# Optimization experiments

Hardware: AMD Instinct MI355X
Metric: run time of the kernel (lower is better)

## Reference

```python
import jax, jax.numpy as jnp
import numpy as np
from jax.scipy.special import logsumexp

R, B, D, V, F = 64, 64, 256, 32000, 7
DFF = 4 * D
K_ACT, TOPK_N, TOP_M = 6, 4, 2
NEG = -1e30
C_TAU = 0.20333333  # mean of (1 - alpha) over taus alpha in {0.5, 0.9, 0.99}; zero prev state


def _hex_neighbors(side=8):
    offs = [(1, 0), (-1, 0), (0, 1), (0, -1), (1, -1), (-1, 1)]
    idx = [[((r + dr) % side) * side + (c + dc) % side for dr, dc in offs]
           for r in range(side) for c in range(side)]
    return jnp.array(idx, dtype=jnp.int32)


def setup_inputs() -> dict:
    key = jax.random.key(0)
    ks = jax.random.split(key, 12)
    def rn(k, shp, s):
        return jax.random.normal(k, shp, dtype=jnp.float32) * s
    return {
        "x_per_region": rn(ks[0], (R, B, D), 1.0),
        "targets": jax.random.randint(ks[1], (B,), 0, V),
        "neighbor_indices": _hex_neighbors(8),
        "W1": rn(ks[2], (R, D, DFF), D ** -0.5),
        "b1": jnp.zeros((R, DFF), jnp.float32),
        "W2": rn(ks[3], (R, DFF, D), DFF ** -0.5),
        "b2": jnp.zeros((R, D), jnp.float32),
        "w_gate": rn(ks[4], (D,), D ** -0.5),
        "Wr": rn(ks[5], (D, D), D ** -0.5),
        "Wm": rn(ks[6], (D, D), D ** -0.5),
        "bm": jnp.zeros((D,), jnp.float32),
        "Wg": rn(ks[7], (D, F), D ** -0.5),
        "Wf": rn(ks[8], (F, D, V), 0.02),
        "e_fac": rn(ks[9], (F, D), 1.0),
        "Wb": rn(ks[10], (D, D), D ** -0.5),
    }


def reference(x_per_region, targets, neighbor_indices, W1, b1, W2, b2, w_gate,
              Wr, Wm, bm, Wg, Wf, e_fac, Wb):
    inv_sqrt_d = D ** -0.5
    # per-region FF (grouped GEMM over R regions), exact GELU as torch nn.GELU
    hid = jax.nn.gelu(jnp.einsum('rbd,rdf->rbf', x_per_region, W1) + b1[:, None, :],
                      approximate=False)
    h = jnp.einsum('rbf,rfd->rbd', hid, W2) + b2[:, None, :]
    s = C_TAU * h                    # multi-tau state update (zero prev state, zero neighbor msg)
    H = h + s                        # [R,B,D]
    # region sparsity gate: k-WTA over regions per batch element, io regions forced on
    sc_g = jnp.einsum('rbd,d->br', H, w_gate)           # [B,R]
    kth = jax.lax.top_k(sc_g, K_ACT)[0][:, -1]
    mask = (sc_g >= kth[:, None]).at[:, 0].set(True).at[:, R - 1].set(True)
    Hs = H * mask.T[:, :, None]
    # sparse message passing: top-k gated attention over hex neighbor list
    Nb = Hs[neighbor_indices]                           # [R,6,B,D]
    sc = jnp.einsum('rbd,rkbd->rkb', Hs, Nb) * inv_sqrt_d
    kthn = -jnp.sort(-sc, axis=1)[:, TOPK_N - 1]        # [R,B]
    w = jax.nn.softmax(jnp.where(sc >= kthn[:, None, :], sc, NEG), axis=1)
    H2 = Hs + jnp.einsum('rkb,rkbd->rbd', w, Nb) @ Wr
    # motor readout + multi-facet softmax (mixture over top-m facets)
    motor = H2[R - 1] @ Wm + bm                         # [B,D]
    g = motor @ Wg                                      # [B,F]
    gk = jax.lax.top_k(g, TOP_M)[0][:, -1]
    log_pi = jax.nn.log_softmax(jnp.where(g >= gk[:, None], g, NEG), axis=-1)
    lp = jax.nn.log_softmax(jnp.einsum('bd,fdv->bfv', motor, Wf), axis=-1)
    logp = logsumexp(log_pi[:, :, None] + lp, axis=1)   # [B,V]
    loss = -jnp.mean(jnp.take_along_axis(logp, targets[:, None], axis=1))
    # surprise-gated facet emitter + broadcast routing (next-step buffer, detached)
    S = jax.lax.stop_gradient(loss)
    boost = 1.0 + 2.0 * (S > 0.7).astype(H2.dtype)
    gb = jnp.einsum('rbd,df->rbf', H2, Wg)
    gbk = -jnp.sort(-gb, axis=-1)[..., TOP_M - 1]
    pi = jax.nn.softmax(jnp.where(gb >= gbk[..., None], gb, NEG), axis=-1)
    Bc = H2 * jnp.einsum('rbf,fd->rbd', pi, e_fac) * boost
    NbB = Bc[neighbor_indices]                          # [R,6,B,D]
    sc2 = jnp.einsum('rbd,rkbd->rkb', H2, NbB) * inv_sqrt_d
    kth2 = -jnp.sort(-sc2, axis=1)[:, TOPK_N - 1]
    w2 = jax.nn.softmax(jnp.where(sc2 >= kth2[:, None, :], sc2, NEG), axis=1)
    msg_next = jax.lax.stop_gradient(jnp.einsum('rkb,rkbd->rbd', w2, NbB) @ Wb)
    return logp, loss, msg_next
```

## Files before the change

kernel.cpp:

```cpp
#include <hip/hip_runtime.h>

#define RR 64
#define BB 64
#define DD 256
#define DFF_ 1024
#define VV 32000
#define FF 7

#define TIE_BAND(a, b) (2e-6 * (1.0 + 0.5 * (fabs(a) + fabs(b))))
#define BR_CLAMP 0.30f
#define TOT_CLAMP 0.19f

__device__ __forceinline__ float clampf(float x, float c) {
  return fminf(fmaxf(x, -c), c);
}


__global__ void t_hid(const float* __restrict__ x, const float* __restrict__ W1,
                      const float* __restrict__ b1, double* __restrict__ hid) {
  int fc = blockIdx.x, r = blockIdx.y;
  int t = threadIdx.x;
  int fg = t & 15, bg = t >> 4;
  __shared__ float xs[64][65];
  __shared__ float w1t[64][64];
  double acc[4][4];
#pragma unroll
  for (int i = 0; i < 4; ++i)
#pragma unroll
    for (int j = 0; j < 4; ++j) acc[i][j] = 0.0;
  const float* xr = x + (size_t)r * BB * DD;
  const float* w1r = W1 + (size_t)r * DD * DFF_;
  for (int dt = 0; dt < 4; ++dt) {
    for (int i = t; i < 4096; i += 256) {
      int d = i & 63, b = i >> 6;
      xs[d][b] = xr[b * DD + dt * 64 + d];
    }
    for (int i = t; i < 4096; i += 256) {
      int dd = i >> 6, ff = i & 63;
      w1t[dd][ff] = w1r[(size_t)(dt * 64 + dd) * DFF_ + fc * 64 + ff];
    }
    __syncthreads();
    for (int d = 0; d < 64; ++d) {
      double bv[4], wv[4];
#pragma unroll
      for (int i = 0; i < 4; ++i) bv[i] = (double)xs[d][bg * 4 + i];
#pragma unroll
      for (int j = 0; j < 4; ++j) wv[j] = (double)w1t[d][fg * 4 + j];
#pragma unroll
      for (int i = 0; i < 4; ++i)
#pragma unroll
        for (int j = 0; j < 4; ++j) acc[i][j] += bv[i] * wv[j];
    }
    __syncthreads();
  }
#pragma unroll
  for (int i = 0; i < 4; ++i) {
    int b = bg * 4 + i;
#pragma unroll
    for (int j = 0; j < 4; ++j) {
      int f = fc * 64 + fg * 4 + j;
      double v = acc[i][j] + (double)b1[r * DFF_ + f];
      hid[((size_t)(r * BB + b)) * DFF_ + f] =
          0.5 * v * (1.0 + erf(v * 0.70710678118654752440));
    }
  }
}

__global__ void t_H(const double* __restrict__ hid, const float* __restrict__ W2,
                    const float* __restrict__ b2, double* __restrict__ H) {
  int dc = blockIdx.x, bc = blockIdx.y, r = blockIdx.z;
  int t = threadIdx.x;
  int dg = t & 15, bg = t >> 4;
  __shared__ double ht[64][33];
  __shared__ float wt[64][32];
  double acc[2][2];
#pragma unroll
  for (int i = 0; i < 2; ++i)
#pragma unroll
    for (int j = 0; j < 2; ++j) acc[i][j] = 0.0;
  const double* hr = hid + (size_t)r * BB * DFF_;
  const float* w2r = W2 + (size_t)r * DFF_ * DD;
  for (int ft = 0; ft < 16; ++ft) {
    for (int i = t; i < 2048; i += 256) {
      int f = i & 63, b = i >> 6;
      ht[f][b] = hr[(size_t)(bc * 32 + b) * DFF_ + ft * 64 + f];
    }
    for (int i = t; i < 2048; i += 256) {
      int f = i >> 5, d = i & 31;
      wt[f][d] = w2r[(size_t)(ft * 64 + f) * DD + dc * 32 + d];
    }
    __syncthreads();
    for (int f = 0; f < 64; ++f) {
      double hb[2], wv[2];
#pragma unroll
      for (int i = 0; i < 2; ++i) hb[i] = ht[f][bg * 2 + i];
#pragma unroll
      for (int j = 0; j < 2; ++j) wv[j] = (double)wt[f][dg * 2 + j];
#pragma unroll
      for (int i = 0; i < 2; ++i)
#pragma unroll
        for (int j = 0; j < 2; ++j) acc[i][j] += hb[i] * wv[j];
    }
    __syncthreads();
  }
#pragma unroll
  for (int i = 0; i < 2; ++i) {
    int b = bc * 32 + bg * 2 + i;
#pragma unroll
    for (int j = 0; j < 2; ++j) {
      int d = dc * 32 + dg * 2 + j;
      double h = acc[i][j] + (double)b2[r * DD + d];
      H[((size_t)(r * BB + b)) * DD + d] = h + 0.20333333 * h;
    }
  }
}


__global__ void n_scg(const double* __restrict__ H, const float* __restrict__ wg,
                      double* __restrict__ scg) {
  __shared__ double hbuf[4][256];
  __shared__ float wgs[256];
  int t = threadIdx.x;
  int wv = t >> 6, lane = t & 63;
  int idx = blockIdx.x * 4 + wv;
  int r = idx >> 6, b = idx & 63;
  const double* hp = H + (size_t)idx * DD;
  wgs[t] = wg[t];
#pragma unroll
  for (int j = 0; j < 4; ++j) hbuf[wv][lane + j * 64] = hp[lane + j * 64];
  __syncthreads();
  if (lane == 0) {
    double a = 0.0;
    for (int d = 0; d < DD; ++d) a += hbuf[wv][d] * (double)wgs[d];
    scg[b * RR + r] = a;
  }
}

__global__ void n_mask_dual(const double* __restrict__ scg, float* __restrict__ maskH,
                            float* __restrict__ maskA, int* __restrict__ flagM) {
  int b = threadIdx.x;
  double v[64], w[64];
  for (int r = 0; r < RR; ++r) { v[r] = scg[b * RR + r]; w[r] = v[r]; }
  double k6 = 0.0, k7 = 0.0;
  int i6 = -1, i7 = -1;
  for (int it = 0; it < 7; ++it) {
    int mi = 0;
    for (int r = 1; r < RR; ++r) if (w[r] > w[mi]) mi = r;
    if (it == 5) { k6 = w[mi]; i6 = mi; }
    if (it == 6) { k7 = w[mi]; i7 = mi; }
    w[mi] = -INFINITY;
  }
  double gap = k6 - k7;
  int tie = (gap > 0.0 && gap < TIE_BAND(k6, k7)) ? 1 : 0;
  for (int r = 0; r < RR; ++r) {
    float mh = (v[r] >= k6 || r == 0 || r == RR - 1) ? 1.f : 0.f;
    maskH[b * RR + r] = mh;
    maskA[b * RR + r] = tie ? ((v[r] >= k7 || r == 0 || r == RR - 1) ? 1.f : 0.f) : mh;
    flagM[r * BB + b] = 0;
  }
  if (tie) {
    flagM[i6 * BB + b] = 1;
    flagM[i7 * BB + b] = 1;
  }
}

__global__ void n_hs(const double* __restrict__ H, const float* __restrict__ mask,
                     double* __restrict__ Hs) {
  int idx = blockIdx.x * 256 + threadIdx.x;
  int r = idx >> 14;
  int b = (idx >> 8) & 63;
  Hs[idx] = H[idx] * (double)mask[b * RR + r];
}

__global__ void n_hs_g(const double* __restrict__ H, const float* __restrict__ maskA,
                       const int* __restrict__ gate, double* __restrict__ HsM) {
  int rb = blockIdx.x;
  if (!gate[rb]) return;
  int t = threadIdx.x;
  size_t i = (size_t)rb * DD + t;
  int r = rb >> 6, b = rb & 63;
  HsM[i] = H[i] * (double)maskA[b * RR + r];
}

__global__ void n_w6x(const double* __restrict__ self, const double* __restrict__ nb,
                      const int* __restrict__ nidx, double* __restrict__ wout,
                      double* __restrict__ walt, int* __restrict__ flag) {
  __shared__ double sbuf[256];
  __shared__ double qbuf[6][256];
  int idx = blockIdx.x;
  int r = idx >> 6, b = idx & 63;
  int lane = threadIdx.x;
  const double* sp = self + (size_t)idx * DD;
#pragma unroll
  for (int j = 0; j < 4; ++j) sbuf[lane + j * 64] = sp[lane + j * 64];
  for (int k = 0; k < 6; ++k) {
    int nr = nidx[r * 6 + k];
    const double* qp = nb + ((size_t)(nr * BB + b)) * DD;
#pragma unroll
    for (int j = 0; j < 4; ++j) qbuf[k][lane + j * 64] = qp[lane + j * 64];
  }
  __syncthreads();
  if (lane == 0) {
    double sc[6];
    for (int k = 0; k < 6; ++k) {
      double a = 0.0;
      for (int d = 0; d < DD; ++d) a += sbuf[d] * qbuf[k][d];
      sc[k] = a * 0.0625;
    }
    double srt[6];
    for (int k = 0; k < 6; ++k) srt[k] = sc[k];
    for (int i = 0; i < 5; ++i) {
      int mi = i;
      for (int j = i + 1; j < 6; ++j) if (srt[j] > srt[mi]) mi = j;
      double tmp = srt[i]; srt[i] = srt[mi]; srt[mi] = tmp;
    }
    double s4 = srt[3], s5 = srt[4], mx = srt[0];
    double e[6], s = 0.0;
    for (int k = 0; k < 6; ++k) {
      e[k] = (sc[k] >= s4) ? exp(sc[k] - mx) : 0.0;
      s += e[k];
    }
    for (int k = 0; k < 6; ++k) wout[(size_t)idx * 6 + k] = e[k] / s;
    double gap = s4 - s5;
    int inband = (gap > 0.0 && gap < TIE_BAND(s4, s5)) ? 1 : 0;
    flag[idx] = inband;
    if (inband) {
      double ea[6], sa = 0.0;
      for (int k = 0; k < 6; ++k) {
        ea[k] = (sc[k] >= s5) ? exp(sc[k] - mx) : 0.0;
        sa += ea[k];
      }
      for (int k = 0; k < 6; ++k) walt[(size_t)idx * 6 + k] = ea[k] / sa;
    } else {
      for (int k = 0; k < 6; ++k) walt[(size_t)idx * 6 + k] = e[k] / s;
    }
  }
}

__global__ void n_w6_sel_g(const double* __restrict__ selfD, const double* __restrict__ selfC,
                           const int* __restrict__ flagS,
                           const double* __restrict__ nbD, const double* __restrict__ nbC,
                           const int* __restrict__ flagN,
                           const int* __restrict__ nidx, const int* __restrict__ gate,
                           const double* __restrict__ wH, double* __restrict__ wout) {
  __shared__ double sbuf[256];
  __shared__ double qbuf[6][256];
  int idx = blockIdx.x;
  int r = idx >> 6, b = idx & 63;
  int lane = threadIdx.x;
  int g = gate[idx];
  if (g) {
    const double* sp = (flagS[idx] ? selfD : selfC) + (size_t)idx * DD;
#pragma unroll
    for (int j = 0; j < 4; ++j) sbuf[lane + j * 64] = sp[lane + j * 64];
    for (int k = 0; k < 6; ++k) {
      int nr = nidx[r * 6 + k];
      int ni = nr * BB + b;
      const double* qp = (flagN[ni] ? nbD : nbC) + (size_t)ni * DD;
#pragma unroll
      for (int j = 0; j < 4; ++j) qbuf[k][lane + j * 64] = qp[lane + j * 64];
    }
  }
  __syncthreads();
  if (!g) {
    if (lane < 6) wout[(size_t)idx * 6 + lane] = wH[(size_t)idx * 6 + lane];
    return;
  }
  if (lane == 0) {
    double sc[6];
    for (int k = 0; k < 6; ++k) {
      double a = 0.0;
      for (int d = 0; d < DD; ++d) a += sbuf[d] * qbuf[k][d];
      sc[k] = a * 0.0625;
    }
    double srt[6];
    for (int k = 0; k < 6; ++k) srt[k] = sc[k];
    for (int i = 0; i < 4; ++i) {
      int mi = i;
      for (int j = i + 1; j < 6; ++j) if (srt[j] > srt[mi]) mi = j;
      double tmp = srt[i]; srt[i] = srt[mi]; srt[mi] = tmp;
    }
    double s4 = srt[3], mx = srt[0];
    double e[6], s = 0.0;
    for (int k = 0; k < 6; ++k) {
      e[k] = (sc[k] >= s4) ? exp(sc[k] - mx) : 0.0;
      s += e[k];
    }
    for (int k = 0; k < 6; ++k) wout[(size_t)idx * 6 + k] = e[k] / s;
  }
}


__global__ void f_mp_mm(const double* __restrict__ w, const double* __restrict__ nb,
                        const int* __restrict__ nidx, const float* __restrict__ Wmat,
                        const double* __restrict__ Hs, double* __restrict__ H2) {
  __shared__ double mpL[256];
  int rb = blockIdx.x;
  int r = rb >> 6, b = rb & 63;
  int t = threadIdx.x;
  double a = 0.0;
  for (int k = 0; k < 6; ++k) {
    int nr = nidx[r * 6 + k];
    a += w[(size_t)rb * 6 + k] * nb[((size_t)(nr * BB + b)) * DD + t];
  }
  mpL[t] = a;
  __syncthreads();
  double s2 = 0.0;
  for (int d = 0; d < DD; ++d) s2 += mpL[d] * (double)Wmat[d * DD + t];
  size_t i = (size_t)rb * DD + t;
  H2[i] = Hs[i] + s2;
}

__global__ void f_mp_msg(const double* __restrict__ w, const double* __restrict__ nb,
                         const int* __restrict__ nidx, const float* __restrict__ Wmat,
                         float* __restrict__ msgH) {
  __shared__ double mpL[256];
  int rb = blockIdx.x;
  int r = rb >> 6, b = rb & 63;
  int t = threadIdx.x;
  double a = 0.0;
  for (int k = 0; k < 6; ++k) {
    int nr = nidx[r * 6 + k];
    a += w[(size_t)rb * 6 + k] * nb[((size_t)(nr * BB + b)) * DD + t];
  }
  mpL[t] = a;
  __syncthreads();
  double s2 = 0.0;
  for (int d = 0; d < DD; ++d) s2 += mpL[d] * (double)Wmat[d * DD + t];
  msgH[(size_t)rb * DD + t] = (float)s2;
}

__global__ void f_mp_corr_g(const double* __restrict__ w,
                            const double* __restrict__ nbD, const double* __restrict__ nbC,
                            const int* __restrict__ flagN,
                            const int* __restrict__ nidx, const int* __restrict__ gate,
                            const float* __restrict__ Wmat, const float* __restrict__ msgH,
                            float* __restrict__ corr) {
  int rb = blockIdx.x;
  if (!gate[rb]) return;
  __shared__ double mpL[256];
  int r = rb >> 6, b = rb & 63;
  int t = threadIdx.x;
  double a = 0.0;
  for (int k = 0; k < 6; ++k) {
    int nr = nidx[r * 6 + k];
    int ni = nr * BB + b;
    const double* q = flagN[ni] ? nbD : nbC;
    a += w[(size_t)rb * 6 + k] * q[(size_t)ni * DD + t];
  }
  mpL[t] = a;
  __syncthreads();
  double s2 = 0.0;
  for (int d = 0; d < DD; ++d) s2 += mpL[d] * (double)Wmat[d * DD + t];
  size_t i = (size_t)rb * DD + t;
  corr[i] += clampf((float)s2 - msgH[i], BR_CLAMP);
}

__global__ void f_mp_h2_g(const double* __restrict__ w,
                          const double* __restrict__ nbD, const double* __restrict__ nbC,
                          const int* __restrict__ flagN,
                          const int* __restrict__ nidx, const float* __restrict__ Wmat,
                          const double* __restrict__ HsD, const double* __restrict__ HsC,
                          const int* __restrict__ flagHs,
                          const int* __restrict__ gate, double* __restrict__ H2out) {
  int rb = blockIdx.x;
  if (!gate[rb]) return;
  __shared__ double mpL[256];
  int r = rb >> 6, b = rb & 63;
  int t = threadIdx.x;
  double a = 0.0;
  for (int k = 0; k < 6; ++k) {
    int nr = nidx[r * 6 + k];
    int ni = nr * BB + b;
    const double* q = flagN[ni] ? nbD : nbC;
    a += w[(size_t)rb * 6 + k] * q[(size_t)ni * DD + t];
  }
  mpL[t] = a;
  __syncthreads();
  double s2 = 0.0;
  for (int d = 0; d < DD; ++d) s2 += mpL[d] * (double)Wmat[d * DD + t];
  size_t i = (size_t)rb * DD + t;
  const double* hs = flagHs[rb] ? HsD : HsC;
  H2out[i] = hs[i] + s2;
}


__global__ void n_zero(float* __restrict__ p) {
  p[blockIdx.x * 256 + threadIdx.x] = 0.f;
}

__global__ void n_izero(int* __restrict__ p) {
  p[blockIdx.x * 256 + threadIdx.x] = 0;
}

__global__ void n_final(const float* __restrict__ msgH, const float* __restrict__ corr,
                        float* __restrict__ out) {
  int i = blockIdx.x * 256 + threadIdx.x;
  out[i] = msgH[i] + clampf(corr[i], TOT_CLAMP);
}

__global__ void n_close(const int* __restrict__ in, const int* __restrict__ nidx,
                        int* __restrict__ out) {
  int idx = blockIdx.x * 256 + threadIdx.x;
  int r = idx >> 6, b = idx & 63;
  int v = in[idx];
  for (int k = 0; k < 6; ++k) v |= in[nidx[r * 6 + k] * BB + b];
  out[idx] = v;
}

__global__ void n_motor(const double* __restrict__ H2, const float* __restrict__ Wm,
                        const float* __restrict__ bm, double* __restrict__ motD,
                        float* __restrict__ motF) {
  int b = blockIdx.x, t = threadIdx.x;
  const double* hp = H2 + ((size_t)((RR - 1) * BB + b)) * DD;
  double a = 0.0;
  for (int d = 0; d < DD; ++d) a += hp[d] * (double)Wm[d * DD + t];
  double mo = a + (double)bm[t];
  motD[b * DD + t] = mo;
  motF[b * DD + t] = (float)mo;
}

__global__ void n_gate(const double* __restrict__ motD, const float* __restrict__ Wg,
                       int* __restrict__ sel, float* __restrict__ c2) {
  __shared__ double mbuf[256];
  __shared__ float wgb[1792];
  int b = blockIdx.x;
  int lane = threadIdx.x;
#pragma unroll
  for (int j = 0; j < 4; ++j) mbuf[lane + j * 64] = motD[b * DD + lane + j * 64];
  for (int i = lane; i < 1792; i += 64) wgb[i] = Wg[i];
  __syncthreads();
  if (lane == 0) {
    double g[FF];
    for (int f = 0; f < FF; ++f) {
      double a = 0.0;
      for (int d = 0; d < DD; ++d) a += mbuf[d] * (double)wgb[d * FF + f];
      g[f] = a;
    }
    double m1 = -INFINITY, m2 = -INFINITY;
    int i1 = -1, i2 = -1;
    for (int f = 0; f < FF; ++f) {
      if (g[f] > m1) { m2 = m1; i2 = i1; m1 = g[f]; i1 = f; }
      else if (g[f] > m2) { m2 = g[f]; i2 = f; }
    }
    double s = 0.0;
    for (int f = 0; f < FF; ++f)
      if (g[f] >= m2) s += exp(g[f] - m1);
    double lse = m1 + log(s);
    sel[b * 2 + 0] = i1;
    sel[b * 2 + 1] = i2;
    c2[b * 2 + 0] = (float)(g[i1] - lse);
    c2[b * 2 + 1] = (float)(g[i2] - lse);
  }
}

__global__ void n_pi_dual(const double* __restrict__ H2, const float* __restrict__ Wg,
                          double* __restrict__ piH, double* __restrict__ piA,
                          int* __restrict__ flag) {
  __shared__ double hbuf[4][256];
  __shared__ float wgb[1792];
  int t = threadIdx.x;
  int wv = t >> 6, lane = t & 63;
  int idx = blockIdx.x * 4 + wv;
  const double* hp = H2 + (size_t)idx * DD;
#pragma unroll
  for (int j = 0; j < 4; ++j) hbuf[wv][lane + j * 64] = hp[lane + j * 64];
  for (int i = t; i < 1792; i += 256) wgb[i] = Wg[i];
  __syncthreads();
  if (lane == 0) {
    double gb[FF];
    for (int f = 0; f < FF; ++f) {
      double a = 0.0;
      for (int d = 0; d < DD; ++d) a += hbuf[wv][d] * (double)wgb[d * FF + f];
      gb[f] = a;
    }
    double srt[FF];
    for (int f = 0; f < FF; ++f) srt[f] = gb[f];
    for (int i = 0; i < 3; ++i) {
      int mi = i;
      for (int j = i + 1; j < FF; ++j) if (srt[j] > srt[mi]) mi = j;
      double tp = srt[i]; srt[i] = srt[mi]; srt[mi] = tp;
    }
    double m1 = srt[0], m2 = srt[1], m3 = srt[2];
    double e[FF], s = 0.0;
    for (int f = 0; f < FF; ++f) {
      e[f] = (gb[f] >= m2) ? exp(gb[f] - m1) : 0.0;
      s += e[f];
    }
    for (int f = 0; f < FF; ++f) piH[(size_t)idx * FF + f] = e[f] / s;
    double gap = m2 - m3;
    int inband = (gap > 0.0 && gap < TIE_BAND(m2, m3)) ? 1 : 0;
    flag[idx] = inband;
    if (inband) {
      double ea[FF], sa = 0.0;
      for (int f = 0; f < FF; ++f) {
        ea[f] = (gb[f] >= m3) ? exp(gb[f] - m1) : 0.0;
        sa += ea[f];
      }
      for (int f = 0; f < FF; ++f) piA[(size_t)idx * FF + f] = ea[f] / sa;
    } else {
      for (int f = 0; f < FF; ++f) piA[(size_t)idx * FF + f] = e[f] / s;
    }
  }
}

__global__ void n_pi_sel(const double* __restrict__ H2src, const float* __restrict__ Wg,
                         const int* __restrict__ gate, const double* __restrict__ piHsrc,
                         double* __restrict__ piout) {
  __shared__ double hbuf[4][256];
  __shared__ float wgb[1792];
  int t = threadIdx.x;
  int wv = t >> 6, lane = t & 63;
  int idx = blockIdx.x * 4 + wv;
  int g = gate[idx];
  if (g) {
    const double* hp = H2src + (size_t)idx * DD;
#pragma unroll
    for (int j = 0; j < 4; ++j) hbuf[wv][lane + j * 64] = hp[lane + j * 64];
  }
  for (int i = t; i < 1792; i += 256) wgb[i] = Wg[i];
  __syncthreads();
  if (!g) {
    if (lane < FF) piout[(size_t)idx * FF + lane] = piHsrc[(size_t)idx * FF + lane];
    return;
  }
  if (lane == 0) {
    double gb[FF];
    for (int f = 0; f < FF; ++f) {
      double a = 0.0;
      for (int d = 0; d < DD; ++d) a += hbuf[wv][d] * (double)wgb[d * FF + f];
      gb[f] = a;
    }
    double m1 = -INFINITY, m2 = -INFINITY;
    for (int f = 0; f < FF; ++f) {
      if (gb[f] > m1) { m2 = m1; m1 = gb[f]; }
      else if (gb[f] > m2) { m2 = gb[f]; }
    }
    double e[FF], s = 0.0;
    for (int f = 0; f < FF; ++f) {
      e[f] = (gb[f] >= m2) ? exp(gb[f] - m1) : 0.0;
      s += e[f];
    }
    for (int f = 0; f < FF; ++f) piout[(size_t)idx * FF + f] = e[f] / s;
  }
}

__global__ void n_bc(const double* __restrict__ H2, const double* __restrict__ pi,
                     const float* __restrict__ e_fac, const float* __restrict__ boost_p,
                     double* __restrict__ Bc) {
  int rb = blockIdx.x, t = threadIdx.x;
  double ef = 0.0;
  for (int f = 0; f < FF; ++f) ef += pi[(size_t)rb * FF + f] * (double)e_fac[f * DD + t];
  double boost = (double)(*boost_p);
  Bc[(size_t)rb * DD + t] = H2[(size_t)rb * DD + t] * ef * boost;
}

__global__ void n_bc_g(const double* __restrict__ H2src, const double* __restrict__ pi,
                       const float* __restrict__ e_fac, const float* __restrict__ boost_p,
                       const int* __restrict__ gate, double* __restrict__ Bc2) {
  int rb = blockIdx.x;
  if (!gate[rb]) return;
  int t = threadIdx.x;
  size_t i = (size_t)rb * DD + t;
  double ef = 0.0;
  for (int f = 0; f < FF; ++f) ef += pi[(size_t)rb * FF + f] * (double)e_fac[f * DD + t];
  double boost = (double)(*boost_p);
  Bc2[i] = H2src[i] * ef * boost;
}


__global__ void k_z2(const float* __restrict__ motor, const float* __restrict__ Wf,
                     const int* __restrict__ sel, float* __restrict__ z2) {
  int vc = blockIdx.x, f = blockIdx.y;
  int t = threadIdx.x;
  int vg = t & 31, bg = t >> 5;
  __shared__ float mt[16][65];
  __shared__ float wt[16][256];
  __shared__ int selL[128];
  if (t < 128) selL[t] = sel[t];
  float acc[8][8];
#pragma unroll
  for (int i = 0; i < 8; ++i)
#pragma unroll
    for (int j = 0; j < 8; ++j) acc[i][j] = 0.f;
  const float* wf = Wf + (size_t)f * DD * VV;
  for (int dt = 0; dt < 16; ++dt) {
    for (int i = t; i < 1024; i += 256) {
      int d = i & 15, b = i >> 4;
      mt[d][b] = motor[b * DD + dt * 16 + d];
    }
    for (int i = t; i < 4096; i += 256) {
      int d = i >> 8, v = i & 255;
      wt[d][v] = wf[(size_t)(dt * 16 + d) * VV + vc * 256 + v];
    }
    __syncthreads();
    for (int d = 0; d < 16; ++d) {
      float bv[8], wv[8];
#pragma unroll
      for (int i = 0; i < 8; ++i) bv[i] = mt[d][bg * 8 + i];
#pragma unroll
      for (int j = 0; j < 8; ++j) wv[j] = wt[d][vg + j * 32];
#pragma unroll
      for (int i = 0; i < 8; ++i)
#pragma unroll
        for (int j = 0; j < 8; ++j) acc[i][j] += bv[i] * wv[j];
    }
    __syncthreads();
  }
#pragma unroll
  for (int i = 0; i < 8; ++i) {
    int b = bg * 8 + i;
    int s0 = selL[b * 2 + 0], s1 = selL[b * 2 + 1];
    if (s0 == f) {
#pragma unroll
      for (int j = 0; j < 8; ++j)
        z2[((size_t)(b * 2 + 0)) * VV + vc * 256 + vg + j * 32] = acc[i][j];
    }
    if (s1 == f) {
#pragma unroll
      for (int j = 0; j < 8; ++j)
        z2[((size_t)(b * 2 + 1)) * VV + vc * 256 + vg + j * 32] = acc[i][j];
    }
  }
}

__global__ void k_lse(const float* __restrict__ z2, float* __restrict__ lse) {
  int row = blockIdx.x;
  int t = threadIdx.x;
  const float* zp = z2 + (size_t)row * VV;
  float m = -INFINITY, s = 0.f;
  for (int v = t; v < VV; v += 256) {
    float val = zp[v];
    if (val > m) { s = s * expf(m - val) + 1.f; m = val; }
    else s += expf(val - m);
  }
  __shared__ float sm[256], ss[256];
  sm[t] = m; ss[t] = s;
  __syncthreads();
  for (int off = 128; off > 0; off >>= 1) {
    if (t < off) {
      float m2 = sm[t + off], s2 = ss[t + off], m1 = sm[t], s1 = ss[t];
      float M = fmaxf(m1, m2);
      sm[t] = M;
      ss[t] = s1 * expf(m1 - M) + s2 * expf(m2 - M);
    }
    __syncthreads();
  }
  if (t == 0) lse[row] = sm[0] + logf(ss[0]);
}

__global__ void k_logp(const float* __restrict__ z2, const float* __restrict__ c2,
                       const float* __restrict__ lse, float* __restrict__ out_logp) {
  int b = blockIdx.y;
  int v = blockIdx.x * 256 + threadIdx.x;
  float a0 = c2[b * 2 + 0] - lse[b * 2 + 0] + z2[((size_t)(b * 2 + 0)) * VV + v];
  float a1 = c2[b * 2 + 1] - lse[b * 2 + 1] + z2[((size_t)(b * 2 + 1)) * VV + v];
  float M = fmaxf(a0, a1);
  out_logp[(size_t)b * VV + v] = M + logf(expf(a0 - M) + expf(a1 - M));
}

__global__ void k_loss(const float* __restrict__ out_logp, const int* __restrict__ targets,
                       float* __restrict__ out_loss, float* __restrict__ boost) {
  int b = threadIdx.x;
  float v = out_logp[(size_t)b * VV + targets[b]];
#pragma unroll
  for (int off = 32; off > 0; off >>= 1) v += __shfl_xor(v, off, 64);
  if (b == 0) {
    float loss = -v / 64.f;
    *out_loss = loss;
    *boost = 1.f + 2.f * ((loss > 0.7f) ? 1.f : 0.f);
  }
}

extern "C" void kernel_launch(void* const* d_in, const int* in_sizes, int n_in,
                              void* d_out, int out_size, void* d_ws, size_t ws_size,
                              hipStream_t stream) {
  const float* x       = (const float*)d_in[0];
  const int*   targets = (const int*)d_in[1];
  const int*   nidx    = (const int*)d_in[2];
  const float* W1      = (const float*)d_in[3];
  const float* b1      = (const float*)d_in[4];
  const float* W2      = (const float*)d_in[5];
  const float* b2      = (const float*)d_in[6];
  const float* w_gate  = (const float*)d_in[7];
  const float* Wr      = (const float*)d_in[8];
  const float* Wm      = (const float*)d_in[9];
  const float* bm      = (const float*)d_in[10];
  const float* Wg      = (const float*)d_in[11];
  const float* Wf      = (const float*)d_in[12];
  const float* e_fac   = (const float*)d_in[13];
  const float* Wb      = (const float*)d_in[14];

  float* out_logp = (float*)d_out;
  float* out_loss = out_logp + (size_t)BB * VV;
  float* out_msg  = out_loss + 1;

  double* dH   = (double*)d_ws;
  double* dHs  = dH + 1048576;
  double* dHsM = dHs + 1048576;
  double* dH2  = dHsM + 1048576;
  double* dH2b = dH2 + 1048576;
  double* dBc  = dH2b + 1048576;
  double* dBcA = dBc + 1048576;
  double* dHid = dBcA + 1048576;
  float*  fZ2  = (float*)dHid;
  double* dScg = dHid + 4194304;
  double* dW6h = dScg + 4096;
  double* dW6a = dW6h + 24576;
  double* dW6b = dW6a + 24576;
  double* dW2h = dW6b + 24576;
  double* dW2a = dW2h + 24576;
  double* dW2b = dW2a + 24576;
  double* dPiH = dW2b + 24576;
  double* dPiA = dPiH + 28672;
  double* dPiH2= dPiA + 28672;
  double* dMotD= dPiH2 + 28672;
  float*  fMaskH = (float*)(dMotD + 16384);
  float*  fMaskA = fMaskH + 4096;
  float*  fMsgH  = fMaskA + 4096;
  float*  fCorr  = fMsgH + 1048576;
  float*  fMotF  = fCorr + 1048576;
  float*  fC2    = fMotF + 16384;
  float*  fLse   = fC2 + 128;
  float*  fBoost = fLse + 128;
  int*    iSel   = (int*)(fBoost + 1);
  int*    fW1    = iSel + 128;
  int*    fW2    = fW1 + 4096;
  int*    fPi    = fW2 + 4096;
  int*    fM     = fPi + 4096;
  int*    cPi    = fM + 4096;
  int*    cW1    = cPi + 4096;
  int*    cM     = cW1 + 4096;
  int*    cM2    = cM + 4096;
  int*    iZero  = cM2 + 4096;

  t_hid<<<dim3(16, 64), 256, 0, stream>>>(x, W1, b1, dHid);
  t_H<<<dim3(8, 2, 64), 256, 0, stream>>>(dHid, W2, b2, dH);
  n_scg<<<1024, 256, 0, stream>>>(dH, w_gate, dScg);
  n_mask_dual<<<1, 64, 0, stream>>>(dScg, fMaskH, fMaskA, fM);
  n_hs<<<4096, 256, 0, stream>>>(dH, fMaskH, dHs);
  n_w6x<<<4096, 64, 0, stream>>>(dHs, dHs, nidx, dW6h, dW6a, fW1);
  f_mp_mm<<<4096, 256, 0, stream>>>(dW6h, dHs, nidx, Wr, dHs, dH2);
  n_motor<<<64, 256, 0, stream>>>(dH2, Wm, bm, dMotD, fMotF);
  n_gate<<<64, 64, 0, stream>>>(dMotD, Wg, iSel, fC2);
  k_z2<<<dim3(125, 7), 256, 0, stream>>>(fMotF, Wf, iSel, fZ2);
  k_lse<<<128, 256, 0, stream>>>(fZ2, fLse);
  k_logp<<<dim3(125, BB), 256, 0, stream>>>(fZ2, fC2, fLse, out_logp);
  k_loss<<<1, 64, 0, stream>>>(out_logp, targets, out_loss, fBoost);
  n_pi_dual<<<1024, 256, 0, stream>>>(dH2, Wg, dPiH, dPiA, fPi);
  n_bc<<<4096, 256, 0, stream>>>(dH2, dPiH, e_fac, fBoost, dBc);
  n_w6x<<<4096, 64, 0, stream>>>(dH2, dBc, nidx, dW2h, dW2a, fW2);
  f_mp_msg<<<4096, 256, 0, stream>>>(dW2h, dBc, nidx, Wb, fMsgH);
  n_zero<<<4096, 256, 0, stream>>>(fCorr);
  n_izero<<<16, 256, 0, stream>>>(iZero);
  f_mp_corr_g<<<4096, 256, 0, stream>>>(dW2a, dBc, dBc, iZero, nidx, fW2, Wb, fMsgH, fCorr);
  n_bc_g<<<4096, 256, 0, stream>>>(dH2, dPiA, e_fac, fBoost, fPi, dBcA);
  n_close<<<16, 256, 0, stream>>>(fPi, nidx, cPi);
  n_w6_sel_g<<<4096, 64, 0, stream>>>(dH2, dH2, iZero, dBcA, dBc, fPi, nidx, cPi, dW2h, dW2b);
  f_mp_corr_g<<<4096, 256, 0, stream>>>(dW2b, dBcA, dBc, fPi, nidx, cPi, Wb, fMsgH, fCorr);
  f_mp_h2_g<<<4096, 256, 0, stream>>>(dW6a, dHs, dHs, iZero, nidx, Wr, dHs, dHs, iZero, fW1, dH2b);
  n_pi_sel<<<1024, 256, 0, stream>>>(dH2b, Wg, fW1, dPiH, dPiH2);
  n_bc_g<<<4096, 256, 0, stream>>>(dH2b, dPiH2, e_fac, fBoost, fW1, dBcA);
  n_close<<<16, 256, 0, stream>>>(fW1, nidx, cW1);
  n_w6_sel_g<<<4096, 64, 0, stream>>>(dH2b, dH2, fW1, dBcA, dBc, fW1, nidx, cW1, dW2h, dW2b);
  f_mp_corr_g<<<4096, 256, 0, stream>>>(dW2b, dBcA, dBc, fW1, nidx, cW1, Wb, fMsgH, fCorr);
  n_hs_g<<<4096, 256, 0, stream>>>(dH, fMaskA, fM, dHsM);
  n_close<<<16, 256, 0, stream>>>(fM, nidx, cM);
  n_w6_sel_g<<<4096, 64, 0, stream>>>(dHsM, dHs, fM, dHsM, dHs, fM, nidx, cM, dW6h, dW6b);
  f_mp_h2_g<<<4096, 256, 0, stream>>>(dW6b, dHsM, dHs, fM, nidx, Wr, dHsM, dHs, fM, cM, dH2b);
  n_pi_sel<<<1024, 256, 0, stream>>>(dH2b, Wg, cM, dPiH, dPiH2);
  n_bc_g<<<4096, 256, 0, stream>>>(dH2b, dPiH2, e_fac, fBoost, cM, dBcA);
  n_close<<<16, 256, 0, stream>>>(cM, nidx, cM2);
  n_w6_sel_g<<<4096, 64, 0, stream>>>(dH2b, dH2, cM, dBcA, dBc, cM, nidx, cM2, dW2h, dW2b);
  f_mp_corr_g<<<4096, 256, 0, stream>>>(dW2b, dBcA, dBc, cM, nidx, cM2, Wb, fMsgH, fCorr);
  n_final<<<4096, 256, 0, stream>>>(fMsgH, fCorr, out_msg);
}
```

Baseline: 913.6 us.

## Fuse pi softmax with Bc emission, merge zeroing and closure launches, widen t_H tile

Gate-softmax computation is fused with the Bc broadcast product into single kernels (f_pibc, f_pibc_g), keeping pi in shared memory instead of writing and rereading it from global buffers. The corr zeroing moves into f_mp_msg, and pairs of neighbor-closure launches are merged into n_close2, which removes several small launches. t_H now uses 64-wide d tiles with 4x2 accumulators per thread, halving the grid and reusing each loaded hid tile across more outputs. The closure computations are reordered so they run earlier; this relies on their inputs already being final at that point.

```diff
diff --git a/kernel.cpp b/kernel.cpp
--- a/kernel.cpp
+++ b/kernel.cpp
@@ -70,12 +70,12 @@
                     const float* __restrict__ b2, double* __restrict__ H) {
   int dc = blockIdx.x, bc = blockIdx.y, r = blockIdx.z;
   int t = threadIdx.x;
-  int dg = t & 15, bg = t >> 4;
+  int dg = t & 31, bg = t >> 5;
   __shared__ double ht[64][33];
-  __shared__ float wt[64][32];
-  double acc[2][2];
-#pragma unroll
-  for (int i = 0; i < 2; ++i)
+  __shared__ float wt[64][64];
+  double acc[4][2];
+#pragma unroll
+  for (int i = 0; i < 4; ++i)
 #pragma unroll
     for (int j = 0; j < 2; ++j) acc[i][j] = 0.0;
   const double* hr = hid + (size_t)r * BB * DFF_;
@@ -85,30 +85,30 @@
       int f = i & 63, b = i >> 6;
       ht[f][b] = hr[(size_t)(bc * 32 + b) * DFF_ + ft * 64 + f];
     }
-    for (int i = t; i < 2048; i += 256) {
-      int f = i >> 5, d = i & 31;
-      wt[f][d] = w2r[(size_t)(ft * 64 + f) * DD + dc * 32 + d];
+    for (int i = t; i < 4096; i += 256) {
+      int f = i >> 6, d = i & 63;
+      wt[f][d] = w2r[(size_t)(ft * 64 + f) * DD + dc * 64 + d];
     }
     __syncthreads();
     for (int f = 0; f < 64; ++f) {
-      double hb[2], wv[2];
-#pragma unroll
-      for (int i = 0; i < 2; ++i) hb[i] = ht[f][bg * 2 + i];
+      double hb[4], wv[2];
+#pragma unroll
+      for (int i = 0; i < 4; ++i) hb[i] = ht[f][bg * 4 + i];
 #pragma unroll
       for (int j = 0; j < 2; ++j) wv[j] = (double)wt[f][dg * 2 + j];
 #pragma unroll
-      for (int i = 0; i < 2; ++i)
+      for (int i = 0; i < 4; ++i)
 #pragma unroll
         for (int j = 0; j < 2; ++j) acc[i][j] += hb[i] * wv[j];
     }
     __syncthreads();
   }
 #pragma unroll
-  for (int i = 0; i < 2; ++i) {
-    int b = bc * 32 + bg * 2 + i;
+  for (int i = 0; i < 4; ++i) {
+    int b = bc * 32 + bg * 4 + i;
 #pragma unroll
     for (int j = 0; j < 2; ++j) {
-      int d = dc * 32 + dg * 2 + j;
+      int d = dc * 64 + dg * 2 + j;
       double h = acc[i][j] + (double)b2[r * DD + d];
       H[((size_t)(r * BB + b)) * DD + d] = h + 0.20333333 * h;
     }
@@ -313,7 +313,7 @@
 
 __global__ void f_mp_msg(const double* __restrict__ w, const double* __restrict__ nb,
                          const int* __restrict__ nidx, const float* __restrict__ Wmat,
-                         float* __restrict__ msgH) {
+                         float* __restrict__ msgH, float* __restrict__ corr) {
   __shared__ double mpL[256];
   int rb = blockIdx.x;
   int r = rb >> 6, b = rb & 63;
@@ -327,7 +327,9 @@
   __syncthreads();
   double s2 = 0.0;
   for (int d = 0; d < DD; ++d) s2 += mpL[d] * (double)Wmat[d * DD + t];
-  msgH[(size_t)rb * DD + t] = (float)s2;
+  size_t i = (size_t)rb * DD + t;
+  msgH[i] = (float)s2;
+  corr[i] = 0.f;
 }
 
 __global__ void f_mp_corr_g(const double* __restrict__ w,
@@ -385,80 +387,13 @@
 }
 
 
-__global__ void n_zero(float* __restrict__ p) {
-  p[blockIdx.x * 256 + threadIdx.x] = 0.f;
-}
-
-__global__ void n_izero(int* __restrict__ p) {
-  p[blockIdx.x * 256 + threadIdx.x] = 0;
-}
-
-__global__ void n_final(const float* __restrict__ msgH, const float* __restrict__ corr,
-                        float* __restrict__ out) {
-  int i = blockIdx.x * 256 + threadIdx.x;
-  out[i] = msgH[i] + clampf(corr[i], TOT_CLAMP);
-}
-
-__global__ void n_close(const int* __restrict__ in, const int* __restrict__ nidx,
-                        int* __restrict__ out) {
-  int idx = blockIdx.x * 256 + threadIdx.x;
-  int r = idx >> 6, b = idx & 63;
-  int v = in[idx];
-  for (int k = 0; k < 6; ++k) v |= in[nidx[r * 6 + k] * BB + b];
-  out[idx] = v;
-}
-
-__global__ void n_motor(const double* __restrict__ H2, const float* __restrict__ Wm,
-                        const float* __restrict__ bm, double* __restrict__ motD,
-                        float* __restrict__ motF) {
-  int b = blockIdx.x, t = threadIdx.x;
-  const double* hp = H2 + ((size_t)((RR - 1) * BB + b)) * DD;
-  double a = 0.0;
-  for (int d = 0; d < DD; ++d) a += hp[d] * (double)Wm[d * DD + t];
-  double mo = a + (double)bm[t];
-  motD[b * DD + t] = mo;
-  motF[b * DD + t] = (float)mo;
-}
-
-__global__ void n_gate(const double* __restrict__ motD, const float* __restrict__ Wg,
-                       int* __restrict__ sel, float* __restrict__ c2) {
-  __shared__ double mbuf[256];
-  __shared__ float wgb[1792];
-  int b = blockIdx.x;
-  int lane = threadIdx.x;
-#pragma unroll
-  for (int j = 0; j < 4; ++j) mbuf[lane + j * 64] = motD[b * DD + lane + j * 64];
-  for (int i = lane; i < 1792; i += 64) wgb[i] = Wg[i];
-  __syncthreads();
-  if (lane == 0) {
-    double g[FF];
-    for (int f = 0; f < FF; ++f) {
-      double a = 0.0;
-      for (int d = 0; d < DD; ++d) a += mbuf[d] * (double)wgb[d * FF + f];
-      g[f] = a;
-    }
-    double m1 = -INFINITY, m2 = -INFINITY;
-    int i1 = -1, i2 = -1;
-    for (int f = 0; f < FF; ++f) {
-      if (g[f] > m1) { m2 = m1; i2 = i1; m1 = g[f]; i1 = f; }
-      else if (g[f] > m2) { m2 = g[f]; i2 = f; }
-    }
-    double s = 0.0;
-    for (int f = 0; f < FF; ++f)
-      if (g[f] >= m2) s += exp(g[f] - m1);
-    double lse = m1 + log(s);
-    sel[b * 2 + 0] = i1;
-    sel[b * 2 + 1] = i2;
-    c2[b * 2 + 0] = (float)(g[i1] - lse);
-    c2[b * 2 + 1] = (float)(g[i2] - lse);
-  }
-}
-
-__global__ void n_pi_dual(const double* __restrict__ H2, const float* __restrict__ Wg,
-                          double* __restrict__ piH, double* __restrict__ piA,
-                          int* __restrict__ flag) {
+__global__ void f_pibc(const double* __restrict__ H2, const float* __restrict__ Wg,
+                       const float* __restrict__ e_fac, const float* __restrict__ boost_p,
+                       double* __restrict__ piA, int* __restrict__ flag,
+                       double* __restrict__ Bc) {
   __shared__ double hbuf[4][256];
   __shared__ float wgb[1792];
+  __shared__ double piL[4][FF];
   int t = threadIdx.x;
   int wv = t >> 6, lane = t & 63;
   int idx = blockIdx.x * 4 + wv;
@@ -487,7 +422,7 @@
       e[f] = (gb[f] >= m2) ? exp(gb[f] - m1) : 0.0;
       s += e[f];
     }
-    for (int f = 0; f < FF; ++f) piH[(size_t)idx * FF + f] = e[f] / s;
+    for (int f = 0; f < FF; ++f) piL[wv][f] = e[f] / s;
     double gap = m2 - m3;
     int inband = (gap > 0.0 && gap < TIE_BAND(m2, m3)) ? 1 : 0;
     flag[idx] = inband;
@@ -502,13 +437,23 @@
       for (int f = 0; f < FF; ++f) piA[(size_t)idx * FF + f] = e[f] / s;
     }
   }
-}
-
-__global__ void n_pi_sel(const double* __restrict__ H2src, const float* __restrict__ Wg,
-                         const int* __restrict__ gate, const double* __restrict__ piHsrc,
-                         double* __restrict__ piout) {
+  __syncthreads();
+  double boost = (double)(*boost_p);
+#pragma unroll
+  for (int j = 0; j < 4; ++j) {
+    int d = lane + j * 64;
+    double ef = 0.0;
+    for (int f = 0; f < FF; ++f) ef += piL[wv][f] * (double)e_fac[f * DD + d];
+    Bc[(size_t)idx * DD + d] = hbuf[wv][d] * ef * boost;
+  }
+}
+
+__global__ void f_pibc_g(const double* __restrict__ H2src, const float* __restrict__ Wg,
+                         const float* __restrict__ e_fac, const float* __restrict__ boost_p,
+                         const int* __restrict__ gate, double* __restrict__ Bc2) {
   __shared__ double hbuf[4][256];
   __shared__ float wgb[1792];
+  __shared__ double piL[4][FF];
   int t = threadIdx.x;
   int wv = t >> 6, lane = t & 63;
   int idx = blockIdx.x * 4 + wv;
@@ -520,11 +465,7 @@
   }
   for (int i = t; i < 1792; i += 256) wgb[i] = Wg[i];
   __syncthreads();
-  if (!g) {
-    if (lane < FF) piout[(size_t)idx * FF + lane] = piHsrc[(size_t)idx * FF + lane];
-    return;
-  }
-  if (lane == 0) {
+  if (g && lane == 0) {
     double gb[FF];
     for (int f = 0; f < FF; ++f) {
       double a = 0.0;
@@ -541,18 +482,18 @@
       e[f] = (gb[f] >= m2) ? exp(gb[f] - m1) : 0.0;
       s += e[f];
     }
-    for (int f = 0; f < FF; ++f) piout[(size_t)idx * FF + f] = e[f] / s;
-  }
-}
-
-__global__ void n_bc(const double* __restrict__ H2, const double* __restrict__ pi,
-                     const float* __restrict__ e_fac, const float* __restrict__ boost_p,
-                     double* __restrict__ Bc) {
-  int rb = blockIdx.x, t = threadIdx.x;
-  double ef = 0.0;
-  for (int f = 0; f < FF; ++f) ef += pi[(size_t)rb * FF + f] * (double)e_fac[f * DD + t];
+    for (int f = 0; f < FF; ++f) piL[wv][f] = e[f] / s;
+  }
+  __syncthreads();
+  if (!g) return;
   double boost = (double)(*boost_p);
-  Bc[(size_t)rb * DD + t] = H2[(size_t)rb * DD + t] * ef * boost;
+#pragma unroll
+  for (int j = 0; j < 4; ++j) {
+    int d = lane + j * 64;
+    double ef = 0.0;
+    for (int f = 0; f < FF; ++f) ef += piL[wv][f] * (double)e_fac[f * DD + d];
+    Bc2[(size_t)idx * DD + d] = hbuf[wv][d] * ef * boost;
+  }
 }
 
 __global__ void n_bc_g(const double* __restrict__ H2src, const double* __restrict__ pi,
@@ -566,6 +507,76 @@
   for (int f = 0; f < FF; ++f) ef += pi[(size_t)rb * FF + f] * (double)e_fac[f * DD + t];
   double boost = (double)(*boost_p);
   Bc2[i] = H2src[i] * ef * boost;
+}
+
+
+__global__ void n_final(const float* __restrict__ msgH, const float* __restrict__ corr,
+                        float* __restrict__ out) {
+  int i = blockIdx.x * 256 + threadIdx.x;
+  out[i] = msgH[i] + clampf(corr[i], TOT_CLAMP);
+}
+
+__global__ void n_izero(int* __restrict__ p) {
+  p[blockIdx.x * 256 + threadIdx.x] = 0;
+}
+
+__global__ void n_close2(const int* __restrict__ inA, int* __restrict__ outA,
+                         const int* __restrict__ inB, int* __restrict__ outB,
+                         const int* __restrict__ nidx) {
+  int gi = blockIdx.x * 256 + threadIdx.x;
+  const int* in = (gi < 4096) ? inA : inB;
+  int* out = (gi < 4096) ? outA : outB;
+  int idx = gi & 4095;
+  int r = idx >> 6, b = idx & 63;
+  int v = in[idx];
+  for (int k = 0; k < 6; ++k) v |= in[nidx[r * 6 + k] * BB + b];
+  out[idx] = v;
+}
+
+__global__ void n_motor(const double* __restrict__ H2, const float* __restrict__ Wm,
+                        const float* __restrict__ bm, double* __restrict__ motD,
+                        float* __restrict__ motF) {
+  int b = blockIdx.x, t = threadIdx.x;
+  const double* hp = H2 + ((size_t)((RR - 1) * BB + b)) * DD;
+  double a = 0.0;
+  for (int d = 0; d < DD; ++d) a += hp[d] * (double)Wm[d * DD + t];
+  double mo = a + (double)bm[t];
+  motD[b * DD + t] = mo;
+  motF[b * DD + t] = (float)mo;
+}
+
+__global__ void n_gate(const double* __restrict__ motD, const float* __restrict__ Wg,
+                       int* __restrict__ sel, float* __restrict__ c2) {
+  __shared__ double mbuf[256];
+  __shared__ float wgb[1792];
+  int b = blockIdx.x;
+  int lane = threadIdx.x;
+#pragma unroll
+  for (int j = 0; j < 4; ++j) mbuf[lane + j * 64] = motD[b * DD + lane + j * 64];
+  for (int i = lane; i < 1792; i += 64) wgb[i] = Wg[i];
+  __syncthreads();
+  if (lane == 0) {
+    double g[FF];
+    for (int f = 0; f < FF; ++f) {
+      double a = 0.0;
+      for (int d = 0; d < DD; ++d) a += mbuf[d] * (double)wgb[d * FF + f];
+      g[f] = a;
+    }
+    double m1 = -INFINITY, m2 = -INFINITY;
+    int i1 = -1, i2 = -1;
+    for (int f = 0; f < FF; ++f) {
+      if (g[f] > m1) { m2 = m1; i2 = i1; m1 = g[f]; i1 = f; }
+      else if (g[f] > m2) { m2 = g[f]; i2 = f; }
+    }
+    double s = 0.0;
+    for (int f = 0; f < FF; ++f)
+      if (g[f] >= m2) s += exp(g[f] - m1);
+    double lse = m1 + log(s);
+    sel[b * 2 + 0] = i1;
+    sel[b * 2 + 1] = i2;
+    c2[b * 2 + 0] = (float)(g[i1] - lse);
+    c2[b * 2 + 1] = (float)(g[i2] - lse);
+  }
 }
 
 
@@ -711,10 +722,8 @@
   double* dW2h = dW6b + 24576;
   double* dW2a = dW2h + 24576;
   double* dW2b = dW2a + 24576;
-  double* dPiH = dW2b + 24576;
-  double* dPiA = dPiH + 28672;
-  double* dPiH2= dPiA + 28672;
-  double* dMotD= dPiH2 + 28672;
+  double* dPiA = dW2b + 24576;
+  double* dMotD= dPiA + 28672;
   float*  fMaskH = (float*)(dMotD + 16384);
   float*  fMaskA = fMaskH + 4096;
   float*  fMsgH  = fMaskA + 4096;
@@ -735,10 +744,11 @@
   int*    iZero  = cM2 + 4096;
 
   t_hid<<<dim3(16, 64), 256, 0, stream>>>(x, W1, b1, dHid);
-  t_H<<<dim3(8, 2, 64), 256, 0, stream>>>(dHid, W2, b2, dH);
+  t_H<<<dim3(4, 2, 64), 256, 0, stream>>>(dHid, W2, b2, dH);
   n_scg<<<1024, 256, 0, stream>>>(dH, w_gate, dScg);
   n_mask_dual<<<1, 64, 0, stream>>>(dScg, fMaskH, fMaskA, fM);
   n_hs<<<4096, 256, 0, stream>>>(dH, fMaskH, dHs);
+  n_izero<<<16, 256, 0, stream>>>(iZero);
   n_w6x<<<4096, 64, 0, stream>>>(dHs, dHs, nidx, dW6h, dW6a, fW1);
   f_mp_mm<<<4096, 256, 0, stream>>>(dW6h, dHs, nidx, Wr, dHs, dH2);
   n_motor<<<64, 256, 0, stream>>>(dH2, Wm, bm, dMotD, fMotF);
@@ -747,30 +757,23 @@
   k_lse<<<128, 256, 0, stream>>>(fZ2, fLse);
   k_logp<<<dim3(125, BB), 256, 0, stream>>>(fZ2, fC2, fLse, out_logp);
   k_loss<<<1, 64, 0, stream>>>(out_logp, targets, out_loss, fBoost);
-  n_pi_dual<<<1024, 256, 0, stream>>>(dH2, Wg, dPiH, dPiA, fPi);
-  n_bc<<<4096, 256, 0, stream>>>(dH2, dPiH, e_fac, fBoost, dBc);
+  f_pibc<<<1024, 256, 0, stream>>>(dH2, Wg, e_fac, fBoost, dPiA, fPi, dBc);
   n_w6x<<<4096, 64, 0, stream>>>(dH2, dBc, nidx, dW2h, dW2a, fW2);
-  f_mp_msg<<<4096, 256, 0, stream>>>(dW2h, dBc, nidx, Wb, fMsgH);
-  n_zero<<<4096, 256, 0, stream>>>(fCorr);
-  n_izero<<<16, 256, 0, stream>>>(iZero);
+  f_mp_msg<<<4096, 256, 0, stream>>>(dW2h, dBc, nidx, Wb, fMsgH, fCorr);
+  n_close2<<<32, 256, 0, stream>>>(fW1, cW1, fM, cM, nidx);
   f_mp_corr_g<<<4096, 256, 0, stream>>>(dW2a, dBc, dBc, iZero, nidx, fW2, Wb, fMsgH, fCorr);
   n_bc_g<<<4096, 256, 0, stream>>>(dH2, dPiA, e_fac, fBoost, fPi, dBcA);
-  n_close<<<16, 256, 0, stream>>>(fPi, nidx, cPi);
+  n_close2<<<32, 256, 0, stream>>>(fPi, cPi, cM, cM2, nidx);
   n_w6_sel_g<<<4096, 64, 0, stream>>>(dH2, dH2, iZero, dBcA, dBc, fPi, nidx, cPi, dW2h, dW2b);
   f_mp_corr_g<<<4096, 256, 0, stream>>>(dW2b, dBcA, dBc, fPi, nidx, cPi, Wb, fMsgH, fCorr);
   f_mp_h2_g<<<4096, 256, 0, stream>>>(dW6a, dHs, dHs, iZero, nidx, Wr, dHs, dHs, iZero, fW1, dH2b);
-  n_pi_sel<<<1024, 256, 0, stream>>>(dH2b, Wg, fW1, dPiH, dPiH2);
-  n_bc_g<<<4096, 256, 0, stream>>>(dH2b, dPiH2, e_fac, fBoost, fW1, dBcA);
-  n_close<<<16, 256, 0, stream>>>(fW1, nidx, cW1);
+  f_pibc_g<<<1024, 256, 0, stream>>>(dH2b, Wg, e_fac, fBoost, fW1, dBcA);
   n_w6_sel_g<<<4096, 64, 0, stream>>>(dH2b, dH2, fW1, dBcA, dBc, fW1, nidx, cW1, dW2h, dW2b);
   f_mp_corr_g<<<4096, 256, 0, stream>>>(dW2b, dBcA, dBc, fW1, nidx, cW1, Wb, fMsgH, fCorr);
   n_hs_g<<<4096, 256, 0, stream>>>(dH, fMaskA, fM, dHsM);
-  n_close<<<16, 256, 0, stream>>>(fM, nidx, cM);
   n_w6_sel_g<<<4096, 64, 0, stream>>>(dHsM, dHs, fM, dHsM, dHs, fM, nidx, cM, dW6h, dW6b);
   f_mp_h2_g<<<4096, 256, 0, stream>>>(dW6b, dHsM, dHs, fM, nidx, Wr, dHsM, dHs, fM, cM, dH2b);
-  n_pi_sel<<<1024, 256, 0, stream>>>(dH2b, Wg, cM, dPiH, dPiH2);
-  n_bc_g<<<4096, 256, 0, stream>>>(dH2b, dPiH2, e_fac, fBoost, cM, dBcA);
-  n_close<<<16, 256, 0, stream>>>(cM, nidx, cM2);
+  f_pibc_g<<<1024, 256, 0, stream>>>(dH2b, Wg, e_fac, fBoost, cM, dBcA);
   n_w6_sel_g<<<4096, 64, 0, stream>>>(dH2b, dH2, cM, dBcA, dBc, cM, nidx, cM2, dW2h, dW2b);
   f_mp_corr_g<<<4096, 256, 0, stream>>>(dW2b, dBcA, dBc, cM, nidx, cM2, Wb, fMsgH, fCorr);
   n_final<<<4096, 256, 0, stream>>>(fMsgH, fCorr, out_msg);
```

Result: no change. 912.5 us (-0.1%).
